# Kernel tuning notes

Measured on AMD Instinct MI355X. Metric: run time of the kernel, lower is better.

Reference implementation:

```python
import jax, jax.numpy as jnp
import numpy as np

EPS = 1e-5
NUM_HEADS = 20


def ln(x, w, b=None):
    m = x.mean(-1, keepdims=True)
    v = x.var(-1, keepdims=True)
    y = (x - m) * jax.lax.rsqrt(v + EPS) * w
    return y + b if b is not None else y


def rotate_half(t):
    t1, t2 = jnp.split(t, 2, axis=-1)
    return jnp.concatenate([-t2, t1], axis=-1)


def setup_inputs() -> dict:
    key = jax.random.key(0)
    B, S, E = 8, 1024, 1280  # 8 packed sequences of length 1024, ESM-2 650M width
    T = B * S
    ks = jax.random.split(key, 6)
    scale = (1.0 / E) ** 0.5  # ~xavier scale
    w = lambda k: jax.random.normal(k, (E, E), jnp.float32) * scale
    return {
        "x": jax.random.normal(ks[0], (T, E), jnp.float32),
        "cu_lens": jnp.arange(B + 1, dtype=jnp.int32) * S,
        "max_len": S,
        "norm_w": jnp.ones((E,), jnp.float32),
        "norm_b": jnp.zeros((E,), jnp.float32),
        "Wq": w(ks[1]),
        "Wk": w(ks[2]),
        "Wv": w(ks[3]),
        "Wout": w(ks[4]),
        "lnq_w": jnp.ones((E,), jnp.float32),
        "lnk_w": jnp.ones((E,), jnp.float32),
    }


def reference(x, cu_lens, max_len, norm_w, norm_b, Wq, Wk, Wv, Wout, lnq_w, lnk_w):
    T, E = x.shape
    H = NUM_HEADS
    D = E // H

    # pre-norm + separate Q/K/V projections (bias=False)
    h = ln(x, norm_w, norm_b)
    q = ln(h @ Wq.T, lnq_w)   # per-head-stack LayerNorm on q (no bias)
    k = ln(h @ Wk.T, lnk_w)
    v = h @ Wv.T

    q = q.reshape(T, H, D)
    k = k.reshape(T, H, D)
    v = v.reshape(T, H, D)

    # rotary embedding: positions restart at each sequence boundary (cu_lens)
    tok = jnp.arange(T)
    seg = jnp.searchsorted(cu_lens, tok, side="right") - 1
    pos = (tok - cu_lens[seg]).astype(jnp.float32)
    inv_freq = 1.0 / (10000.0 ** (jnp.arange(0, D, 2, dtype=jnp.float32) / D))
    f = pos[:, None] * inv_freq[None, :]                      # [T, D/2]
    cos = jnp.concatenate([jnp.cos(f), jnp.cos(f)], -1)[:, None, :]  # [T,1,D]
    sin = jnp.concatenate([jnp.sin(f), jnp.sin(f)], -1)[:, None, :]
    q = q * cos + rotate_half(q) * sin
    k = k * cos + rotate_half(k) * sin

    # varlen flash attention; sequences are equal-length here so reshape to
    # [B,S,...] which exactly honors the block-diagonal (no cross-sequence) mask
    B = cu_lens.shape[0] - 1
    S = T // B
    qb = q.reshape(B, S, H, D)
    kb = k.reshape(B, S, H, D)
    vb = v.reshape(B, S, H, D)

    scores = jnp.einsum("bqhd,bkhd->bhqk", qb, kb) * (D ** -0.5)
    attn = jax.nn.softmax(scores, axis=-1)
    o = jnp.einsum("bhqk,bkhd->bqhd", attn, vb).reshape(T, E)
    return o @ Wout.T
```

## Files before the change

### kernel.cpp

```cpp
#include <hip/hip_runtime.h>
#include <hip/hip_bf16.h>
#include <math.h>

#define NH 20
#define HD 64
#define E_DIM 1280
#define T_TOK 8192
#define NSEQ 8
#define N4 (E_DIM * E_DIM / 4)

#define SCALE_LOG2 0.1803368801111204f

typedef unsigned short u16;
typedef unsigned int u32;
typedef __attribute__((ext_vector_type(8))) short bf16x8;
typedef __attribute__((ext_vector_type(4))) float f32x4;
typedef __attribute__((ext_vector_type(16))) float f32x16;

__device__ __forceinline__ float bf2f(u16 h) {
  union { float f; unsigned u; } c; c.u = ((unsigned)h) << 16; return c.f;
}
__device__ __forceinline__ u16 f2bf(float f) {
  union { float f; unsigned u; } c; c.f = f;
  unsigned u = c.u;
  return (u16)((u + 0x7fffu + ((u >> 16) & 1u)) >> 16);
}
__device__ __forceinline__ u32 cvtpk(float lo, float hi) {
  u32 r;
  asm("v_cvt_pk_bf16_f32 %0, %1, %2" : "=v"(r) : "v"(lo), "v"(hi));
  return r;
}

__device__ __forceinline__ void gld_lds16(const void* g, void* l) {
  __builtin_amdgcn_global_load_lds((const __attribute__((address_space(1))) void*)g,
                                   (__attribute__((address_space(3))) void*)l,
                                   16, 0, 0);
}

#define BARR() __builtin_amdgcn_s_barrier()
#define VMC2() asm volatile("s_waitcnt vmcnt(2)" ::: "memory")
#define VMC4() asm volatile("s_waitcnt vmcnt(4)" ::: "memory")
#define VMC0() asm volatile("s_waitcnt vmcnt(0)" ::: "memory")

__global__ __launch_bounds__(256) void cvt_all(const float* __restrict__ Wq,
                                               const float* __restrict__ Wk,
                                               const float* __restrict__ Wv,
                                               const float* __restrict__ Wo,
                                               u16* __restrict__ wqkv,
                                               u16* __restrict__ wo) {
  int i = blockIdx.x * 256 + threadIdx.x;
  if (i >= 4 * N4) return;
  int r = i / N4;
  int l = i - r * N4;
  const float* src = (r == 0) ? Wq : (r == 1) ? Wk : (r == 2) ? Wv : Wo;
  float4 v = ((const float4*)src)[l];
  ushort4 ov;
  ov.x = f2bf(v.x); ov.y = f2bf(v.y); ov.z = f2bf(v.z); ov.w = f2bf(v.w);
  if (r < 3) ((ushort4*)wqkv)[(size_t)r * N4 + l] = ov;
  else       ((ushort4*)wo)[l] = ov;
}

__global__ __launch_bounds__(256) void rope_tab_kernel(float2* __restrict__ tab) {
  int i = blockIdx.x * 256 + threadIdx.x;
  if (i >= 1024 * 32) return;
  int pos = i >> 5, dm = i & 31;
  float freq = exp2f(-(float)dm * (13.287712379549449f / 32.0f));
  float f = (float)pos * freq;
  tab[i] = make_float2(cosf(f), sinf(f));
}

__global__ __launch_bounds__(320) void ln_x_kernel(const float* __restrict__ x,
                                                   const float* __restrict__ w,
                                                   const float* __restrict__ b,
                                                   u16* __restrict__ h) {
  const int row = blockIdx.x;
  const int tid = threadIdx.x;
  const float4 xv = ((const float4*)(x + (size_t)row * E_DIM))[tid];
  float s  = xv.x + xv.y + xv.z + xv.w;
  float s2 = xv.x*xv.x + xv.y*xv.y + xv.z*xv.z + xv.w*xv.w;
#pragma unroll
  for (int m = 1; m < 64; m <<= 1) { s += __shfl_xor(s, m); s2 += __shfl_xor(s2, m); }
  __shared__ float ss[5], ss2[5];
  if ((tid & 63) == 0) { ss[tid >> 6] = s; ss2[tid >> 6] = s2; }
  __syncthreads();
  s  = ss[0] + ss[1] + ss[2] + ss[3] + ss[4];
  s2 = ss2[0] + ss2[1] + ss2[2] + ss2[3] + ss2[4];
  const float mean = s * (1.0f / E_DIM);
  const float var  = s2 * (1.0f / E_DIM) - mean * mean;
  const float rstd = rsqrtf(var + 1e-5f);
  const float4 wv = ((const float4*)w)[tid];
  const float4 bv = ((const float4*)b)[tid];
  ushort4 o;
  o.x = f2bf((xv.x - mean) * rstd * wv.x + bv.x);
  o.y = f2bf((xv.y - mean) * rstd * wv.y + bv.y);
  o.z = f2bf((xv.z - mean) * rstd * wv.z + bv.z);
  o.w = f2bf((xv.w - mean) * rstd * wv.w + bv.w);
  ((ushort4*)(h + (size_t)row * E_DIM))[tid] = o;
}

__global__ __launch_bounds__(320) void ln_rope2_kernel(const u16* __restrict__ preq,
                                                       const u16* __restrict__ prek,
                                                       const float* __restrict__ wq,
                                                       const float* __restrict__ wk,
                                                       const int* __restrict__ cu,
                                                       const float2* __restrict__ tab,
                                                       u16* __restrict__ outq,
                                                       u16* __restrict__ outk) {
  const int sel = blockIdx.x >> 13;
  const int row = blockIdx.x & (T_TOK - 1);
  const u16* pre = sel ? prek : preq;
  const float* w = sel ? wk : wq;
  u16* outp = sel ? outk : outq;
  const float oscale = sel ? 1.0f : SCALE_LOG2;
  const int tid = threadIdx.x;
  __shared__ float y[E_DIM];
  const ushort4 qv = ((const ushort4*)(pre + (size_t)row * E_DIM))[tid];
  float v0 = bf2f(qv.x), v1 = bf2f(qv.y), v2 = bf2f(qv.z), v3 = bf2f(qv.w);
  float s  = v0 + v1 + v2 + v3;
  float s2 = v0*v0 + v1*v1 + v2*v2 + v3*v3;
#pragma unroll
  for (int m = 1; m < 64; m <<= 1) { s += __shfl_xor(s, m); s2 += __shfl_xor(s2, m); }
  __shared__ float ss[5], ss2[5];
  if ((tid & 63) == 0) { ss[tid >> 6] = s; ss2[tid >> 6] = s2; }
  __syncthreads();
  s  = ss[0] + ss[1] + ss[2] + ss[3] + ss[4];
  s2 = ss2[0] + ss2[1] + ss2[2] + ss2[3] + ss2[4];
  const float mean = s * (1.0f / E_DIM);
  const float var  = s2 * (1.0f / E_DIM) - mean * mean;
  const float rstd = rsqrtf(var + 1e-5f);
  const int e0 = tid * 4;
  float4 wv = ((const float4*)w)[tid];
  wv.x *= oscale; wv.y *= oscale; wv.z *= oscale; wv.w *= oscale;
  y[e0 + 0] = (v0 - mean) * rstd * wv.x;
  y[e0 + 1] = (v1 - mean) * rstd * wv.y;
  y[e0 + 2] = (v2 - mean) * rstd * wv.z;
  y[e0 + 3] = (v3 - mean) * rstd * wv.w;
  __syncthreads();
  int seg = 0;
#pragma unroll
  for (int bb = 1; bb < NSEQ + 1; bb++) if (cu[bb] <= row) seg = bb;
  const int pos = row - cu[seg];
  const int d0 = e0 & 63;
  const int hbase = e0 - d0;
  const float4* tp = (const float4*)(tab + pos * 32 + (d0 & 31));
  const float4 t0 = tp[0], t1 = tp[1];
  const float cs_[4] = {t0.x, t0.z, t1.x, t1.z};
  const float sn_[4] = {t0.y, t0.w, t1.y, t1.w};
  const bool lo = (d0 < 32);
  ushort4 o;
#pragma unroll
  for (int i = 0; i < 4; i++) {
    const int d = d0 + i;
    float r;
    if (lo) r = y[hbase + d] * cs_[i] - y[hbase + d + 32] * sn_[i];
    else    r = y[hbase + d] * cs_[i] + y[hbase + d - 32] * sn_[i];
    ((u16*)&o)[i] = f2bf(r);
  }
  ((ushort4*)(outp + (size_t)row * E_DIM))[tid] = o;
}

template <int MODE, int K>
__global__ __launch_bounds__(512) void gemm256(const u16* __restrict__ A,
                                               const u16* __restrict__ B,
                                               u16* __restrict__ preq,
                                               u16* __restrict__ prek,
                                               u16* __restrict__ vT,
                                               float* __restrict__ Cf) {
  __shared__ u16 As[2][16384];
  __shared__ u16 Bs[2][16384];
  const int tid = threadIdx.x;
  const int wid = tid >> 6, lane = tid & 63;
  const int l16 = lane & 15, lq = lane >> 4;
  const int wm = wid >> 2, wn = wid & 3;
  const int bm = blockIdx.x & 31;
  const int bn = blockIdx.x >> 5;
  const int m0 = bm << 8, n0 = bn << 8;
  const int sw = l16 & 7;

  const int row0 = tid >> 3;
  const int ch0 = ((tid & 7) ^ (row0 & 7)) << 3;
  const u16* Abase = A + (size_t)(m0 + row0) * K + ch0;
  const u16* Bbase = B + (size_t)(n0 + row0) * K + ch0;
  const int dst0 = tid * 8;

  const int CA = (wm * 128 + l16) * 64;
  const int CB = (wn * 64 + l16) * 64;
  const int ch_0 = ((0 | lq) ^ sw) << 3;
  const int ch_1 = ((4 | lq) ^ sw) << 3;

  f32x4 acc[8][4] = {};
  bf16x8 aF[4][2], bF[2][2][2];

#define STG(Larr, bufp, hh, gbase, kt) do {                                     \
    const u16* g_ = (gbase) + (size_t)(hh) * 128 * K + (size_t)(kt) * 64;       \
    gld_lds16(g_, &Larr[bufp][(hh) * 8192 + dst0]);                             \
    gld_lds16(g_ + (size_t)64 * K, &Larr[bufp][(hh) * 8192 + dst0 + 4096]);     \
  } while (0)

#define RDA(bufp, a) do {                                                       \
    _Pragma("unroll") for (int mb = 0; mb < 4; mb++) {                          \
      aF[mb][0] = *(const bf16x8*)(&As[bufp][CA + (a) * 4096 + mb * 1024 + ch_0]); \
      aF[mb][1] = *(const bf16x8*)(&As[bufp][CA + (a) * 4096 + mb * 1024 + ch_1]); \
    } } while (0)

#define RDB(bufp, b) do {                                                       \
    _Pragma("unroll") for (int nb = 0; nb < 2; nb++) {                          \
      bF[b][nb][0] = *(const bf16x8*)(&Bs[bufp][CB + (b) * 2048 + nb * 1024 + ch_0]); \
      bF[b][nb][1] = *(const bf16x8*)(&Bs[bufp][CB + (b) * 2048 + nb * 1024 + ch_1]); \
    } } while (0)

#define MFQ(a, b) do {                                                          \
    __builtin_amdgcn_s_setprio(1);                                              \
    _Pragma("unroll") for (int mb = 0; mb < 4; mb++)                            \
    _Pragma("unroll") for (int nb = 0; nb < 2; nb++)                            \
    _Pragma("unroll") for (int kk = 0; kk < 2; kk++)                            \
      acc[(a) * 4 + mb][(b) * 2 + nb] = __builtin_amdgcn_mfma_f32_16x16x32_bf16( \
          aF[mb][kk], bF[b][nb][kk], acc[(a) * 4 + mb][(b) * 2 + nb], 0, 0, 0); \
    __builtin_amdgcn_s_setprio(0); } while (0)

  STG(Bs, 0, 0, Bbase, 0);
  STG(As, 0, 0, Abase, 0);
  STG(Bs, 0, 1, Bbase, 0);
  STG(As, 0, 1, Abase, 0);
  STG(Bs, 1, 0, Bbase, 1);
  STG(As, 1, 0, Abase, 1);
  VMC4();
  BARR();

  const int NIT = K / 128;
  for (int i = 0; i < NIT; i++) {
    const bool lastI = (i == NIT - 1);
    const int k1 = 2 * i + 1, k2 = 2 * i + 2, k3 = 2 * i + 3;
    RDA(0, 0); RDB(0, 0);
    STG(Bs, 1, 1, Bbase, k1);
    MFQ(0, 0); BARR();
    RDB(0, 1);
    STG(As, 1, 1, Abase, k1);
    MFQ(0, 1); BARR();
    RDA(0, 1);
    if (!lastI) STG(Bs, 0, 0, Bbase, k2);
    MFQ(1, 0);
    if (!lastI) VMC2(); else VMC0();
    BARR();
    if (!lastI) STG(As, 0, 0, Abase, k2);
    MFQ(1, 1); BARR();
    RDA(1, 0); RDB(1, 0);
    if (!lastI) STG(Bs, 0, 1, Bbase, k2);
    MFQ(0, 0); BARR();
    RDB(1, 1);
    if (!lastI) STG(As, 0, 1, Abase, k2);
    MFQ(0, 1); BARR();
    RDA(1, 1);
    if (!lastI) STG(Bs, 1, 0, Bbase, k3);
    MFQ(1, 0);
    if (!lastI) VMC2();
    BARR();
    if (!lastI) {
      STG(As, 1, 0, Abase, k3);
      MFQ(1, 1); BARR();
    } else {
      MFQ(1, 1);
    }
  }
#undef STG
#undef RDA
#undef RDB
#undef MFQ

  if (MODE == 0) {
    if (n0 < 2560) {
      u16* dst; int c0;
      if (n0 < 1280) { dst = preq; c0 = n0; }
      else           { dst = prek; c0 = n0 - 1280; }
#pragma unroll
      for (int mi = 0; mi < 8; mi++)
#pragma unroll
        for (int j = 0; j < 4; j++) {
          const size_t rowo = (size_t)(m0 + wm * 128 + mi * 16 + lq * 4 + j) * E_DIM;
#pragma unroll
          for (int ni = 0; ni < 4; ni++)
            dst[rowo + c0 + wn * 64 + ni * 16 + l16] = f2bf(acc[mi][ni][j]);
        }
    } else {
      const int c0 = n0 - 2560;
#pragma unroll
      for (int mi = 0; mi < 8; mi++)
#pragma unroll
        for (int ni = 0; ni < 4; ni++) {
          ushort4 pkt;
          pkt.x = f2bf(acc[mi][ni][0]); pkt.y = f2bf(acc[mi][ni][1]);
          pkt.z = f2bf(acc[mi][ni][2]); pkt.w = f2bf(acc[mi][ni][3]);
          const size_t off = (size_t)(c0 + wn * 64 + ni * 16 + l16) * T_TOK +
                             (m0 + wm * 128 + mi * 16 + lq * 4);
          *(ushort4*)(vT + off) = pkt;
        }
    }
  } else {
#pragma unroll
    for (int mi = 0; mi < 8; mi++)
#pragma unroll
      for (int j = 0; j < 4; j++) {
        const size_t rowo = (size_t)(m0 + wm * 128 + mi * 16 + lq * 4 + j) * E_DIM;
#pragma unroll
        for (int ni = 0; ni < 4; ni++)
          Cf[rowo + n0 + wn * 64 + ni * 16 + l16] = acc[mi][ni][j];
      }
  }
}

__global__ __launch_bounds__(256) void attn_kernel(const u16* __restrict__ q,
                                                   const u16* __restrict__ k,
                                                   const u16* __restrict__ vT,
                                                   const int* __restrict__ cu,
                                                   u16* __restrict__ o) {
  const int bx = blockIdx.x;
  const int hb = bx % (NH * NSEQ);
  const int qt = bx / (NH * NSEQ);
  const int hh = hb % NH;
  const int b  = hb / NH;
  const int base = cu[b];
  const int nkt  = (cu[b + 1] - base) >> 6;
  const int tid  = threadIdx.x;
  const int wid  = tid >> 6, lane = tid & 63;
  const int l31  = lane & 31, hi = lane >> 5;

  __shared__ u16 Ks[2][64 * 64];
  __shared__ u16 Vs[2][64 * 64];

  const int qrow = base + qt * 128 + wid * 32 + l31;
  bf16x8 qf[4];
#pragma unroll
  for (int kk = 0; kk < 4; kk++)
    qf[kk] = *(const bf16x8*)(q + (size_t)qrow * E_DIM + hh * 64 + kk * 16 + hi * 8);

  f32x16 acc0 = {}, acc1 = {};
  float lrow = 0.f;

  const int r0 = tid >> 3;
  const int chs = tid & 7;
  const int cs0 = (chs ^ (r0 & 7)) << 3;
  const int r1 = r0 + 32;
  const int cs1 = (chs ^ (r1 & 7)) << 3;
  const u16* kg0 = k  + (size_t)(base + r0) * E_DIM + hh * 64 + cs0;
  const u16* kg1 = k  + (size_t)(base + r1) * E_DIM + hh * 64 + cs1;
  const u16* vg0 = vT + (size_t)(hh * 64 + r0) * T_TOK + base + cs0;
  const u16* vg1 = vT + (size_t)(hh * 64 + r1) * T_TOK + base + cs1;
  const int ldsoff = wid * 512;

  gld_lds16(kg0, &Ks[0][ldsoff]);
  gld_lds16(kg1, &Ks[0][2048 + ldsoff]);
  gld_lds16(vg0, &Vs[0][ldsoff]);
  gld_lds16(vg1, &Vs[0][2048 + ldsoff]);
  __syncthreads();

  int cur = 0;
  for (int kt = 0; kt < nkt; kt++) {
    if (kt + 1 < nkt) {
      const size_t ko = (size_t)(kt + 1) * 64 * E_DIM;
      const int vo = (kt + 1) * 64;
      u16* kd = Ks[cur ^ 1];
      u16* vd = Vs[cur ^ 1];
      gld_lds16(kg0 + ko, kd + ldsoff);
      gld_lds16(kg1 + ko, kd + 2048 + ldsoff);
      gld_lds16(vg0 + vo, vd + ldsoff);
      gld_lds16(vg1 + vo, vd + 2048 + ldsoff);
    }
    const u16* Kc = Ks[cur];
    const u16* Vc = Vs[cur];

    f32x16 S0 = {}, S1 = {};
#pragma unroll
    for (int kk = 0; kk < 4; kk++) {
      const int c0 = (((kk << 1) | hi) ^ (l31 & 7)) << 3;
      const bf16x8 kf0 = *(const bf16x8*)(Kc + l31 * 64 + c0);
      const bf16x8 kf1 = *(const bf16x8*)(Kc + (32 + l31) * 64 + c0);
      S0 = __builtin_amdgcn_mfma_f32_32x32x16_bf16(kf0, qf[kk], S0, 0, 0, 0);
      S1 = __builtin_amdgcn_mfma_f32_32x32x16_bf16(kf1, qf[kk], S1, 0, 0, 0);
    }

    float rs0 = 0.f, rs1 = 0.f, rs2 = 0.f, rs3 = 0.f;
#pragma unroll
    for (int r = 0; r < 16; r += 4) {
      S0[r + 0] = exp2f(S0[r + 0]); S0[r + 1] = exp2f(S0[r + 1]);
      S0[r + 2] = exp2f(S0[r + 2]); S0[r + 3] = exp2f(S0[r + 3]);
      rs0 += S0[r + 0]; rs1 += S0[r + 1]; rs2 += S0[r + 2]; rs3 += S0[r + 3];
    }
#pragma unroll
    for (int r = 0; r < 16; r += 4) {
      S1[r + 0] = exp2f(S1[r + 0]); S1[r + 1] = exp2f(S1[r + 1]);
      S1[r + 2] = exp2f(S1[r + 2]); S1[r + 3] = exp2f(S1[r + 3]);
      rs0 += S1[r + 0]; rs1 += S1[r + 1]; rs2 += S1[r + 2]; rs3 += S1[r + 3];
    }
    float rs = (rs0 + rs1) + (rs2 + rs3);
    rs += __shfl_xor(rs, 32);
    lrow += rs;

    u32 pw[4][4];
#pragma unroll
    for (int ks = 0; ks < 4; ks++) {
      const int g = (ks & 1) << 3;
      u32 A0, A1, B0, B1;
      if (ks < 2) {
        A0 = cvtpk(S0[g + 0], S0[g + 1]); A1 = cvtpk(S0[g + 2], S0[g + 3]);
        B0 = cvtpk(S0[g + 4], S0[g + 5]); B1 = cvtpk(S0[g + 6], S0[g + 7]);
      } else {
        A0 = cvtpk(S1[g + 0], S1[g + 1]); A1 = cvtpk(S1[g + 2], S1[g + 3]);
        B0 = cvtpk(S1[g + 4], S1[g + 5]); B1 = cvtpk(S1[g + 6], S1[g + 7]);
      }
      asm("v_permlane32_swap_b32 %0, %1" : "+v"(A0), "+v"(B0));
      asm("v_permlane32_swap_b32 %0, %1" : "+v"(A1), "+v"(B1));
      pw[ks][0] = A0; pw[ks][1] = A1; pw[ks][2] = B0; pw[ks][3] = B1;
    }

#pragma unroll
    for (int ks = 0; ks < 4; ks++) {
      const bf16x8 pa = *(const bf16x8*)&pw[ks][0];
      const int c0 = (((ks << 1) | hi) ^ (l31 & 7)) << 3;
      const bf16x8 vf0 = *(const bf16x8*)(Vc + l31 * 64 + c0);
      const bf16x8 vf1 = *(const bf16x8*)(Vc + (32 + l31) * 64 + c0);
      acc0 = __builtin_amdgcn_mfma_f32_32x32x16_bf16(pa, vf0, acc0, 0, 0, 0);
      acc1 = __builtin_amdgcn_mfma_f32_32x32x16_bf16(pa, vf1, acc1, 0, 0, 0);
    }
    __syncthreads();
    cur ^= 1;
  }

  const float linv = 1.0f / lrow;
  const int tok0 = base + qt * 128 + wid * 32;
#pragma unroll
  for (int r = 0; r < 16; r++) {
    const int qr = (r & 3) + 8 * (r >> 2) + 4 * hi;
    const float ls = __shfl(linv, qr);
    const size_t ro = (size_t)(tok0 + qr) * E_DIM + hh * 64 + l31;
    o[ro]      = f2bf(acc0[r] * ls);
    o[ro + 32] = f2bf(acc1[r] * ls);
  }
}

extern "C" void kernel_launch(void* const* d_in, const int* in_sizes, int n_in,
                              void* d_out, int out_size, void* d_ws, size_t ws_size,
                              hipStream_t stream) {
  const float* x      = (const float*)d_in[0];
  const int*   cu     = (const int*)d_in[1];
  const float* norm_w = (const float*)d_in[3];
  const float* norm_b = (const float*)d_in[4];
  const float* Wq     = (const float*)d_in[5];
  const float* Wk     = (const float*)d_in[6];
  const float* Wv     = (const float*)d_in[7];
  const float* Wo     = (const float*)d_in[8];
  const float* lnq    = (const float*)d_in[9];
  const float* lnk    = (const float*)d_in[10];
  float* out = (float*)d_out;

  const size_t EE2 = (size_t)E_DIM * E_DIM * 2;
  const size_t TE2 = (size_t)T_TOK * E_DIM * 2;
  char* p = (char*)d_ws;
  u16* wqkv = (u16*)p; p += 3 * EE2;
  u16* wo_b = (u16*)p; p += EE2;
  u16* h_b  = (u16*)p; p += TE2;
  u16* preq = (u16*)p; p += TE2;
  u16* prek = (u16*)p; p += TE2;
  u16* vT_b = (u16*)p; p += TE2;
  float2* tab = (float2*)p; p += 1024 * 32 * sizeof(float2);

  cvt_all<<<(4 * N4 + 255) / 256, 256, 0, stream>>>(Wq, Wk, Wv, Wo, wqkv, wo_b);
  rope_tab_kernel<<<128, 256, 0, stream>>>(tab);
  ln_x_kernel<<<T_TOK, 320, 0, stream>>>(x, norm_w, norm_b, h_b);

  gemm256<0, E_DIM><<<480, 512, 0, stream>>>(h_b, wqkv, preq, prek, vT_b, nullptr);

  ln_rope2_kernel<<<2 * T_TOK, 320, 0, stream>>>(preq, prek, lnq, lnk, cu, tab, preq, prek);

  attn_kernel<<<8 * NH * NSEQ, 256, 0, stream>>>(preq, prek, vT_b, cu, h_b);

  gemm256<1, E_DIM><<<160, 512, 0, stream>>>(h_b, wo_b, nullptr, nullptr, nullptr, out);
}
```

Measured before the change: 254.3 us.

## Double-buffer GEMM register fragments to overlap LDS reads with MFMA

Splits the A/B register fragments into even/odd sets so the next fragment's LDS reads are issued before the current MFMA block, rather than being serialized in front of it. This hides LDS read latency behind matrix-core work inside the projection GEMM main loop. It costs extra VGPRs for the duplicated fragments, which could lower occupancy or cause spills, and it changes the read/barrier ordering, which has to stay consistent with the LDS buffer reuse.

```diff
diff --git a/kernel.cpp b/kernel.cpp
--- a/kernel.cpp
+++ b/kernel.cpp
@@ -189,7 +189,7 @@
   const int ch_1 = ((4 | lq) ^ sw) << 3;
 
   f32x4 acc[8][4] = {};
-  bf16x8 aF[4][2], bF[2][2][2];
+  bf16x8 aFe[4][2], aFo[4][2], bFe[2][2], bFo[2][2];
 
 #define STG(Larr, bufp, hh, gbase, kt) do {                                     \
     const u16* g_ = (gbase) + (size_t)(hh) * 128 * K + (size_t)(kt) * 64;       \
@@ -197,25 +197,25 @@
     gld_lds16(g_ + (size_t)64 * K, &Larr[bufp][(hh) * 8192 + dst0 + 4096]);     \
   } while (0)
 
-#define RDA(bufp, a) do {                                                       \
+#define RDA_(dst, bufp, a) do {                                                 \
     _Pragma("unroll") for (int mb = 0; mb < 4; mb++) {                          \
-      aF[mb][0] = *(const bf16x8*)(&As[bufp][CA + (a) * 4096 + mb * 1024 + ch_0]); \
-      aF[mb][1] = *(const bf16x8*)(&As[bufp][CA + (a) * 4096 + mb * 1024 + ch_1]); \
+      dst[mb][0] = *(const bf16x8*)(&As[bufp][CA + (a) * 4096 + mb * 1024 + ch_0]); \
+      dst[mb][1] = *(const bf16x8*)(&As[bufp][CA + (a) * 4096 + mb * 1024 + ch_1]); \
     } } while (0)
 
-#define RDB(bufp, b) do {                                                       \
+#define RDB_(dst, bufp, b) do {                                                 \
     _Pragma("unroll") for (int nb = 0; nb < 2; nb++) {                          \
-      bF[b][nb][0] = *(const bf16x8*)(&Bs[bufp][CB + (b) * 2048 + nb * 1024 + ch_0]); \
-      bF[b][nb][1] = *(const bf16x8*)(&Bs[bufp][CB + (b) * 2048 + nb * 1024 + ch_1]); \
+      dst[nb][0] = *(const bf16x8*)(&Bs[bufp][CB + (b) * 2048 + nb * 1024 + ch_0]); \
+      dst[nb][1] = *(const bf16x8*)(&Bs[bufp][CB + (b) * 2048 + nb * 1024 + ch_1]); \
     } } while (0)
 
-#define MFQ(a, b) do {                                                          \
+#define MFQ_(af, bf, a, b) do {                                                 \
     __builtin_amdgcn_s_setprio(1);                                              \
     _Pragma("unroll") for (int mb = 0; mb < 4; mb++)                            \
     _Pragma("unroll") for (int nb = 0; nb < 2; nb++)                            \
     _Pragma("unroll") for (int kk = 0; kk < 2; kk++)                            \
       acc[(a) * 4 + mb][(b) * 2 + nb] = __builtin_amdgcn_mfma_f32_16x16x32_bf16( \
-          aF[mb][kk], bF[b][nb][kk], acc[(a) * 4 + mb][(b) * 2 + nb], 0, 0, 0); \
+          af[mb][kk], bf[nb][kk], acc[(a) * 4 + mb][(b) * 2 + nb], 0, 0, 0);    \
     __builtin_amdgcn_s_setprio(0); } while (0)
 
   STG(Bs, 0, 0, Bbase, 0);
@@ -226,46 +226,47 @@
   STG(As, 1, 0, Abase, 1);
   VMC4();
   BARR();
+  RDA_(aFe, 0, 0); RDB_(bFe, 0, 0);
 
   const int NIT = K / 128;
   for (int i = 0; i < NIT; i++) {
     const bool lastI = (i == NIT - 1);
     const int k1 = 2 * i + 1, k2 = 2 * i + 2, k3 = 2 * i + 3;
-    RDA(0, 0); RDB(0, 0);
     STG(Bs, 1, 1, Bbase, k1);
-    MFQ(0, 0); BARR();
-    RDB(0, 1);
+    RDB_(bFo, 0, 1);
+    MFQ_(aFe, bFe, 0, 0); BARR();
     STG(As, 1, 1, Abase, k1);
-    MFQ(0, 1); BARR();
-    RDA(0, 1);
+    RDA_(aFo, 0, 1);
+    MFQ_(aFe, bFo, 0, 1); BARR();
     if (!lastI) STG(Bs, 0, 0, Bbase, k2);
-    MFQ(1, 0);
+    MFQ_(aFo, bFe, 1, 0);
     if (!lastI) VMC2(); else VMC0();
     BARR();
     if (!lastI) STG(As, 0, 0, Abase, k2);
-    MFQ(1, 1); BARR();
-    RDA(1, 0); RDB(1, 0);
+    RDA_(aFe, 1, 0); RDB_(bFe, 1, 0);
+    MFQ_(aFo, bFo, 1, 1); BARR();
     if (!lastI) STG(Bs, 0, 1, Bbase, k2);
-    MFQ(0, 0); BARR();
-    RDB(1, 1);
+    RDB_(bFo, 1, 1);
+    MFQ_(aFe, bFe, 0, 0); BARR();
     if (!lastI) STG(As, 0, 1, Abase, k2);
-    MFQ(0, 1); BARR();
-    RDA(1, 1);
+    RDA_(aFo, 1, 1);
+    MFQ_(aFe, bFo, 0, 1); BARR();
     if (!lastI) STG(Bs, 1, 0, Bbase, k3);
-    MFQ(1, 0);
+    MFQ_(aFo, bFe, 1, 0);
     if (!lastI) VMC2();
     BARR();
     if (!lastI) {
       STG(As, 1, 0, Abase, k3);
-      MFQ(1, 1); BARR();
+      RDA_(aFe, 0, 0); RDB_(bFe, 0, 0);
+      MFQ_(aFo, bFo, 1, 1); BARR();
     } else {
-      MFQ(1, 1);
+      MFQ_(aFo, bFo, 1, 1);
     }
   }
 #undef STG
-#undef RDA
-#undef RDB
-#undef MFQ
+#undef RDA_
+#undef RDB_
+#undef MFQ_
 
   if (MODE == 0) {
     if (n0 < 2560) {
```

Result: slower. 270.1 us (+6.2%).
